# Kernel tuning notes

Hardware: AMD Instinct MI355X
Metric: run time of the kernel (lower is better)

## Reference

```python
import jax, jax.numpy as jnp
from jax import lax
import numpy as np

B, P, G, C = 16, 6000, 128, 10
PC_MIN = np.array([-54.0, -54.0, -5.0], np.float32)
PC_MAX = np.array([54.0, 54.0, 3.0], np.float32)
CENTER_RADIUS = 1.5
CANDIDATE_TOPK = 5
NUM_HEADS = 6
CLS_W, ALPHA, GAMMA = 2.0, 0.25, 2.0
REG_W, IOU_W = 0.25, 0.25
EPS = 1e-12
INF1, INF2 = 10000.0, 100000.0


def _aabb(boxes):
    # boxes: (N,7) [cx,cy,cz,dx,dy,dz,yaw] -> AABB (min,max) of the 8 rotated corners
    c, d, yaw = boxes[:, :3], boxes[:, 3:6], boxes[:, 6]
    ca, sa = jnp.abs(jnp.cos(yaw)), jnp.abs(jnp.sin(yaw))
    hx = 0.5 * (d[:, 0] * ca + d[:, 1] * sa)
    hy = 0.5 * (d[:, 0] * sa + d[:, 1] * ca)
    h = jnp.stack([hx, hy, 0.5 * d[:, 2]], -1)
    return c - h, c + h


def _iou3d(pred7, gt7):
    # axis-aligned 3D IoU over corner AABBs (reference stand-in for rotated BboxOverlaps3D)
    pmin, pmax = _aabb(pred7)
    gmin, gmax = _aabb(gt7)
    lo = jnp.maximum(pmin[:, None], gmin[None])   # (P,G,3)
    hi = jnp.minimum(pmax[:, None], gmax[None])
    inter = jnp.prod(jnp.maximum(hi - lo, 0.0), -1)
    vp = jnp.prod(pmax - pmin, -1)
    vg = jnp.prod(gmax - gmin, -1)
    return inter / (vp[:, None] + vg[None] - inter + 1e-7)


def _cost_matrix(pred_logits, pred_boxes, gt_boxes, gt_labels):
    # --- focal classification cost ---
    p = jax.nn.sigmoid(pred_logits)                                  # (P,C)
    neg = -jnp.log(1.0 - p + EPS) * (1.0 - ALPHA) * p ** GAMMA
    pos = -jnp.log(p + EPS) * ALPHA * (1.0 - p) ** GAMMA
    cls_cost = (pos - neg)[:, gt_labels] * CLS_W                     # (P,G)

    gt_norm = jnp.concatenate([gt_boxes[:, :3], jnp.log(gt_boxes[:, 3:6]),
                               jnp.sin(gt_boxes[:, 6:7]), jnp.cos(gt_boxes[:, 6:7])], -1)  # (G,8)
    reg_cost = jnp.abs(pred_boxes[:, None, :8] - gt_norm[None]).sum(-1) * REG_W

    # --- IoU cost on denormalized pred boxes ---
    yaw = jnp.arctan2(pred_boxes[:, 6], pred_boxes[:, 7])
    pred7 = jnp.concatenate([pred_boxes[:, :3], jnp.exp(pred_boxes[:, 3:6]), yaw[:, None]], -1)
    ious = _iou3d(pred7, gt_boxes)                                   # (P,G)
    iou_cost = -ious * IOU_W

    # --- in-gt-box / in-center geometric prior ---
    ctr = pred_boxes[:, :3]
    gmin, gmax = _aabb(gt_boxes)
    in_box = jnp.all((ctr[:, None] > gmin[None]) & (ctr[:, None] < gmax[None]), -1)  # (P,G)
    gc, gd = gt_boxes[:, :3], gt_boxes[:, 3:6]
    lo = gc - CENTER_RADIUS * gd
    hi = gc + CENTER_RADIUS * gd
    in_ctr = jnp.all((ctr[:, None] > lo[None]) & (ctr[:, None] < hi[None]), -1)
    valid = jnp.any(in_box, 1) | jnp.any(in_ctr, 1)                  # (P,)
    in_both = in_box & in_ctr

    cost = cls_cost + reg_cost + iou_cost + (~in_both).astype(cls_cost.dtype) * 100.0
    cost = cost + (~valid).astype(cls_cost.dtype)[:, None] * INF1
    return cost, ious, valid


def _assign(pred_logits, pred_boxes, gt_boxes, gt_labels, head_idx):
    cost, ious, valid = _cost_matrix(pred_logits, pred_boxes, gt_boxes, gt_labels)

    # dynamic-k per gt: sum of top-k ious minus head-schedule offset, truncated, min 1
    k = min(CANDIDATE_TOPK, P)
    topk_ious = lax.top_k(ious.T, k)[0]                              # (G,k)
    dyn = jnp.maximum((topk_ious.sum(1) - 0.5 * (NUM_HEADS - head_idx)).astype(jnp.int32), 1)

    # per-gt lowest-cost top-dyn selection via double argsort ranks
    ranks = jnp.argsort(jnp.argsort(cost, axis=0), axis=0)           # (P,G)
    matching = (ranks < dyn[None, :]).astype(cost.dtype)

    # priors matched to >1 gt: keep only the min-cost gt
    prior_mask = matching.sum(1) > 1
    onehot_min = jax.nn.one_hot(jnp.argmin(cost, 1), G, dtype=cost.dtype)
    matching = jnp.where(prior_mask[:, None], onehot_min, matching)

    rows = jnp.arange(P)

    def cond(s):
        i, cst, m = s
        return jnp.any(m.sum(0) == 0) & (i < G + 8)

    def body(s):
        i, cst, m = s
        cst = cst + (m.sum(1) > 0).astype(cst.dtype)[:, None] * INF2
        unmatched = m.sum(0) == 0                                    # (G,)
        pos = jnp.argmin(cst, 0)                                     # (G,) best prior per gt
        m = jnp.where((rows[:, None] == pos[None]) & unmatched[None], 1.0, m)
        over = jnp.any(m.sum(1) > 1)
        oh = jax.nn.one_hot(jnp.argmin(cst, 1), G, dtype=cst.dtype)
        m = jnp.where(over & prior_mask[:, None], oh, m)             # stale mask, as in torch source
        return i + 1, cst, m

    _, _, matching = lax.while_loop(cond, body, (jnp.int32(0), cost, matching))

    fg = matching.sum(1) > 0                                         # (P,) foreground mask
    matched = jnp.where(fg, jnp.argmax(matching, 1), -1).astype(jnp.int32)
    return fg, matched


def setup_inputs():
    key = jax.random.key(0)
    k1, k2, k3, k4, k5, k6, k7, k8 = jax.random.split(key, 8)
    pred_logits = jax.random.normal(k1, (B, P, C), jnp.float32)
    ctr = jax.random.uniform(k2, (B, P, 3), jnp.float32, jnp.array(PC_MIN), jnp.array(PC_MAX))
    logsz = jnp.log(jax.random.uniform(k3, (B, P, 3), jnp.float32, 1.0, 4.0))
    ang = jax.random.uniform(k4, (B, P, 1), jnp.float32, -np.pi, np.pi)
    vel = jax.random.normal(k5, (B, P, 2), jnp.float32)
    pred_boxes = jnp.concatenate([ctr, logsz, jnp.sin(ang), jnp.cos(ang), vel], -1)
    gctr = jax.random.uniform(k6, (B, G, 3), jnp.float32, jnp.array(PC_MIN), jnp.array(PC_MAX))
    gsz = jax.random.uniform(k7, (B, G, 3), jnp.float32, 1.0, 5.0)
    gyaw = jax.random.uniform(k8, (B, G, 1), jnp.float32, -np.pi, np.pi)
    gt_boxes = jnp.concatenate([gctr, gsz, gyaw], -1)
    gt_labels = jax.random.randint(jax.random.fold_in(key, 99), (B, G), 0, C)
    return {"pred_logits": pred_logits, "pred_boxes": pred_boxes,
            "gt_boxes": gt_boxes, "gt_labels": gt_labels, "head_idx": 5}


def reference(pred_logits, pred_boxes, gt_boxes, gt_labels, head_idx):
    f = lambda pl, pb, gb, gl: _assign(pl, pb, gb, gl, head_idx)
    fg, matched = jax.vmap(f)(pred_logits, pred_boxes, gt_boxes, gt_labels)
    return fg, matched
```

## Files before the change

### kernel.cpp

```cpp
#include <hip/hip_runtime.h>
#include <stdint.h>
#include <math.h>

#define NB 16
#define NP 6000
#define NG 128
#define NC 10
#define SELMAX 4
#define GSTR 24
#define PCH 2048
#define NCH 3
#define CPB 2
#define QITER 32
#define EPIW 128

typedef unsigned long long u64;
#define NBPs ((size_t)NB * NP)

__device__ __forceinline__ uint32_t fkey(float f) {
  uint32_t u = __float_as_uint(f);
  return (u & 0x80000000u) ? ~u : (u | 0x80000000u);
}
__device__ __forceinline__ float fkey_inv(uint32_t k) {
  uint32_t u = (k & 0x80000000u) ? (k & 0x7fffffffu) : ~k;
  return __uint_as_float(u);
}
__device__ __forceinline__ u64 shfl_xor_u64(u64 v, int m) {
  uint32_t lo = (uint32_t)v, hi = (uint32_t)(v >> 32);
  lo = (uint32_t)__shfl_xor((int)lo, m, 64);
  hi = (uint32_t)__shfl_xor((int)hi, m, 64);
  return ((u64)hi << 32) | lo;
}
__device__ __forceinline__ u64 block_min_u64(u64 v, u64* sred, int lane, int wid) {
  for (int o = 1; o < 64; o <<= 1) {
    u64 t = shfl_xor_u64(v, o);
    if (t < v) v = t;
  }
  __syncthreads();
  if (lane == 0) sred[wid] = v;
  __syncthreads();
  u64 r = sred[0];
  if (sred[1] < r) r = sred[1];
  if (sred[2] < r) r = sred[2];
  if (sred[3] < r) r = sred[3];
  return r;
}

__global__ __launch_bounds__(256) void prep_kernel(
    const float* __restrict__ gt_boxes,
    const int* __restrict__ gt_labels,
    const float* __restrict__ pred_logits,
    const float* __restrict__ pred_boxes,
    float* __restrict__ gtaux,
    float* __restrict__ paux,
    float* __restrict__ clst,
    int* __restrict__ rowcnt,
    int* __restrict__ rowassign,
    int* __restrict__ colcnt,
    int* __restrict__ wcount) {
#pragma clang fp contract(off)
  __shared__ float shg[NG * 12];
  const int b = blockIdx.y, tid = threadIdx.x;
  if (tid < NG) {
    const int g = tid;
    const float* gb = gt_boxes + ((size_t)b * NG + g) * 7;
    float cx = gb[0], cy = gb[1], cz = gb[2];
    float dx = gb[3], dy = gb[4], dz = gb[5];
    float yaw = gb[6];
    float cyw = cosf(yaw), syw = sinf(yaw);
    float ca = fabsf(cyw), sa = fabsf(syw);
    float hx = 0.5f * (dx * ca + dy * sa);
    float hy = 0.5f * (dx * sa + dy * ca);
    float hz = 0.5f * dz;
    float gmin0 = cx - hx, gmin1 = cy - hy, gmin2 = cz - hz;
    float gmax0 = cx + hx, gmax1 = cy + hy, gmax2 = cz + hz;
    float* s = &shg[g * 12];
    s[0] = gmin0; s[1] = gmin1; s[2] = gmin2;
    s[3] = gmax0; s[4] = gmax1; s[5] = gmax2;
    s[6] = cx - 1.5f * dx; s[7] = cy - 1.5f * dy; s[8] = cz - 1.5f * dz;
    s[9] = cx + 1.5f * dx; s[10] = cy + 1.5f * dy; s[11] = cz + 1.5f * dz;
    if (blockIdx.x == 0) {
      float vg = ((gmax0 - gmin0) * (gmax1 - gmin1)) * (gmax2 - gmin2);
      float* o = gtaux + ((size_t)b * NG + g) * GSTR;
      o[0] = gmin0; o[1] = gmin1; o[2] = gmin2;
      o[3] = gmax0; o[4] = gmax1; o[5] = gmax2;
      o[6] = s[6]; o[7] = s[7]; o[8] = s[8];
      o[9] = s[9]; o[10] = s[10]; o[11] = s[11];
      o[12] = cx; o[13] = cy; o[14] = cz;
      o[15] = logf(dx); o[16] = logf(dy); o[17] = logf(dz);
      o[18] = syw; o[19] = cyw;
      o[20] = vg;
      o[21] = __int_as_float(gt_labels[(size_t)b * NG + g]);
      o[22] = 0.0f; o[23] = 0.0f;
      colcnt[b * NG + g] = 0;
      if (b == 0 && g == 0) wcount[0] = 0;
    }
  }
  __syncthreads();
  const int p = blockIdx.x * 256 + tid;
  if (p >= NP) return;
  const size_t idx = (size_t)b * NP + p;
  const float* lg = pred_logits + idx * NC;
  for (int c = 0; c < NC; ++c) {
    float x = lg[c];
    float pr = 1.0f / (1.0f + expf(-x));
    float neg = (-logf(1.0f - pr + 1e-12f) * 0.75f) * (pr * pr);
    float pos = (-logf(pr + 1e-12f) * 0.25f) * ((1.0f - pr) * (1.0f - pr));
    clst[(size_t)c * NBPs + idx] = (pos - neg) * 2.0f;
  }
  const float* bx = pred_boxes + idx * 10;
  float b0 = bx[0], b1 = bx[1], b2 = bx[2], b3 = bx[3], b4 = bx[4];
  float b5 = bx[5], b6 = bx[6], b7 = bx[7];
  float yaw = atan2f(b6, b7);
  float d0 = expf(b3), d1 = expf(b4), d2 = expf(b5);
  float ca = fabsf(cosf(yaw)), sa = fabsf(sinf(yaw));
  float hx = 0.5f * (d0 * ca + d1 * sa);
  float hy = 0.5f * (d0 * sa + d1 * ca);
  float hz = 0.5f * d2;
  float pmin0 = b0 - hx, pmin1 = b1 - hy, pmin2 = b2 - hz;
  float pmax0 = b0 + hx, pmax1 = b1 + hy, pmax2 = b2 + hz;
  int valid = 0;
  for (int g = 0; g < NG; ++g) {
    const float* s = &shg[g * 12];
    bool inb = (b0 > s[0]) && (b0 < s[3]) && (b1 > s[1]) && (b1 < s[4]) &&
               (b2 > s[2]) && (b2 < s[5]);
    bool inc = (b0 > s[6]) && (b0 < s[9]) && (b1 > s[7]) && (b1 < s[10]) &&
               (b2 > s[8]) && (b2 < s[11]);
    if (inb || inc) { valid = 1; break; }
  }
  float* o = paux + idx * 16;
  o[0] = b0; o[1] = b1; o[2] = b2; o[3] = b3;
  o[4] = b4; o[5] = b5; o[6] = b6; o[7] = b7;
  o[8] = pmin0; o[9] = pmin1; o[10] = pmin2;
  o[11] = pmax0; o[12] = pmax1; o[13] = pmax2;
  o[14] = ((pmax0 - pmin0) * (pmax1 - pmin1)) * (pmax2 - pmin2);
  o[15] = valid ? 0.0f : 10000.0f;
  rowcnt[idx] = 0;
  rowassign[idx] = 0x7fffffff;
}

struct GTp {
  float gmin0, gmin1, gmin2, gmax0, gmax1, gmax2;
  float lo0, lo1, lo2, hi0, hi1, hi2;
  float gtn0, gtn1, gtn2, gtn3, gtn4, gtn5, gtn6, gtn7;
  float vg;
  int label;
};
__device__ __forceinline__ GTp load_gt(const float* __restrict__ gtaux,
                                       int b, int g) {
  const float* ga = gtaux + ((size_t)b * NG + g) * GSTR;
  GTp t;
  t.gmin0 = ga[0]; t.gmin1 = ga[1]; t.gmin2 = ga[2];
  t.gmax0 = ga[3]; t.gmax1 = ga[4]; t.gmax2 = ga[5];
  t.lo0 = ga[6]; t.lo1 = ga[7]; t.lo2 = ga[8];
  t.hi0 = ga[9]; t.hi1 = ga[10]; t.hi2 = ga[11];
  t.gtn0 = ga[12]; t.gtn1 = ga[13]; t.gtn2 = ga[14]; t.gtn3 = ga[15];
  t.gtn4 = ga[16]; t.gtn5 = ga[17]; t.gtn6 = ga[18]; t.gtn7 = ga[19];
  t.vg = ga[20];
  t.label = __float_as_int(ga[21]);
  return t;
}

__device__ __forceinline__ float cost_base(
    float b0, float b1, float b2, float b3, float b4, float b5, float b6,
    float b7, float pmin0, float pmin1, float pmin2, float pmax0, float pmax1,
    float pmax2, float vp, float cls, const GTp& t, float* iou_out) {
#pragma clang fp contract(off)
  float r = fabsf(b0 - t.gtn0);
  r = r + fabsf(b1 - t.gtn1);
  r = r + fabsf(b2 - t.gtn2);
  r = r + fabsf(b3 - t.gtn3);
  r = r + fabsf(b4 - t.gtn4);
  r = r + fabsf(b5 - t.gtn5);
  r = r + fabsf(b6 - t.gtn6);
  r = r + fabsf(b7 - t.gtn7);
  float reg = r * 0.25f;
  float li0 = fmaxf(pmin0, t.gmin0), li1 = fmaxf(pmin1, t.gmin1),
        li2 = fmaxf(pmin2, t.gmin2);
  float hj0 = fminf(pmax0, t.gmax0), hj1 = fminf(pmax1, t.gmax1),
        hj2 = fminf(pmax2, t.gmax2);
  float e0 = fmaxf(hj0 - li0, 0.0f), e1 = fmaxf(hj1 - li1, 0.0f),
        e2 = fmaxf(hj2 - li2, 0.0f);
  float inter = (e0 * e1) * e2;
  float iou = inter / (((vp + t.vg) - inter) + 1e-7f);
  bool inb = (b0 > t.gmin0) && (b0 < t.gmax0) && (b1 > t.gmin1) &&
             (b1 < t.gmax1) && (b2 > t.gmin2) && (b2 < t.gmax2);
  bool inc = (b0 > t.lo0) && (b0 < t.hi0) && (b1 > t.lo1) && (b1 < t.hi1) &&
             (b2 > t.lo2) && (b2 < t.hi2);
  *iou_out = iou;
  return ((cls + reg) + (-(iou * 0.25f))) + ((inb && inc) ? 0.0f : 100.0f);
}

__global__ __launch_bounds__(256) void stage1_kernel(
    const float* __restrict__ paux,
    const float* __restrict__ clst,
    const float* __restrict__ gtaux,
    float* __restrict__ iou5,
    u64* __restrict__ ck) {
#pragma clang fp contract(off)
  const int n = blockIdx.x;
  const int orig = (n & 7) * 384 + (n >> 3);
  const int b = orig / 192;
  const int rem = orig - b * 192;
  const int gq = rem / NCH;
  const int ch = rem - gq * NCH;
  const int g0 = gq * CPB;
  const int tid = threadIdx.x;
  const int lane = tid & 63, wid = tid >> 6;

  __shared__ uint32_t kiouL[CPB][PCH];
  __shared__ uint32_t kcostL[CPB][PCH];

  GTp t0 = load_gt(gtaux, b, g0);
  GTp t1 = load_gt(gtaux, b, g0 + 1);
  const size_t rowbase = (size_t)b * NP;
  const uint32_t PAD_I = fkey(-INFINITY);
  const uint32_t PAD_C = fkey(INFINITY);

  for (int j = 0; j < PCH / 256; ++j) {
    const int pl = j * 256 + tid;
    const int p = ch * PCH + pl;
    uint32_t ki0 = PAD_I, ki1 = PAD_I, kc0 = PAD_C, kc1 = PAD_C;
    if (p < NP) {
      const size_t idx = rowbase + p;
      const float4* pa = (const float4*)(paux + idx * 16);
      float4 A = pa[0], B = pa[1], C = pa[2], D = pa[3];
      float cls0 = clst[(size_t)t0.label * NBPs + idx];
      float cls1 = clst[(size_t)t1.label * NBPs + idx];
      float iou0, iou1;
      float c0 = cost_base(A.x, A.y, A.z, A.w, B.x, B.y, B.z, B.w,
                           C.x, C.y, C.z, C.w, D.x, D.y, D.z,
                           cls0, t0, &iou0);
      float c1 = cost_base(A.x, A.y, A.z, A.w, B.x, B.y, B.z, B.w,
                           C.x, C.y, C.z, C.w, D.x, D.y, D.z,
                           cls1, t1, &iou1);
      ki0 = fkey(iou0); kc0 = fkey(c0 + D.w);
      ki1 = fkey(iou1); kc1 = fkey(c1 + D.w);
    }
    kiouL[0][pl] = ki0;
    kiouL[1][pl] = ki1;
    kcostL[0][pl] = kc0;
    kcostL[1][pl] = kc1;
  }
  __syncthreads();

  const int c = wid >> 1;
  const int col = b * NG + g0 + c;
  const unsigned gbase = (unsigned)(ch * PCH);

  if ((wid & 1) == 0) {
    uint32_t a0 = 0, a1 = 0, a2 = 0, a3 = 0, a4 = 0;
    for (int q = 0; q < QITER; ++q) {
      uint32_t k = kiouL[c][q * 64 + lane];
      if (k > a4) {
        a4 = k;
        if (a4 > a3) { uint32_t t = a4; a4 = a3; a3 = t; }
        if (a3 > a2) { uint32_t t = a3; a3 = a2; a2 = t; }
        if (a2 > a1) { uint32_t t = a2; a2 = a1; a1 = t; }
        if (a1 > a0) { uint32_t t = a1; a1 = a0; a0 = t; }
      }
    }
    int hp = 0;
    for (int k = 0; k < 5; ++k) {
      uint32_t cand = (hp == 0) ? a0 : (hp == 1) ? a1 : (hp == 2) ? a2
                    : (hp == 3) ? a3 : (hp == 4) ? a4 : 0u;
      u64 key = ((u64)cand << 32) | (unsigned)lane;
      u64 r = key;
      for (int o = 1; o < 64; o <<= 1) {
        u64 t = shfl_xor_u64(r, o);
        if (t > r) r = t;
      }
      if (lane == 0)
        iou5[(size_t)col * 16 + ch * 5 + k] = fkey_inv((uint32_t)(r >> 32));
      if (r == key) hp++;
    }
  } else {
    u64 c0 = ~0ull, c1 = ~0ull, c2 = ~0ull, c3 = ~0ull;
    for (int q = 0; q < QITER; ++q) {
      const int pl = q * 64 + lane;
      u64 key = ((u64)kcostL[c][pl] << 32) | (u64)(gbase + (unsigned)pl);
      if (key < c3) {
        c3 = key;
        if (c3 < c2) { u64 t = c3; c3 = c2; c2 = t; }
        if (c2 < c1) { u64 t = c2; c2 = c1; c1 = t; }
        if (c1 < c0) { u64 t = c1; c1 = c0; c0 = t; }
      }
    }
    int hp = 0;
    for (int k = 0; k < 4; ++k) {
      u64 cand = (hp == 0) ? c0 : (hp == 1) ? c1 : (hp == 2) ? c2
               : (hp == 3) ? c3 : ~0ull;
      u64 r = cand;
      for (int o = 1; o < 64; o <<= 1) {
        u64 t = shfl_xor_u64(r, o);
        if (t < r) r = t;
      }
      if (lane == 0) ck[(size_t)col * 16 + ch * 4 + k] = r;
      if (r == cand) hp++;
    }
  }
}

__global__ __launch_bounds__(256) void stage2_kernel(
    const float* __restrict__ iou5,
    const u64* __restrict__ ck,
    const int* __restrict__ head_ptr,
    int* __restrict__ colsel,
    int* __restrict__ rowcnt,
    int* __restrict__ rowassign,
    int* __restrict__ wlist,
    int* __restrict__ wcount) {
#pragma clang fp contract(off)
  const int col = blockIdx.x * 256 + threadIdx.x;
  if (col >= NB * NG) return;
  const int b = col / NG, g = col - b * NG;
  const float* ip = iou5 + (size_t)col * 16;
  float m0 = -INFINITY, m1 = -INFINITY, m2 = -INFINITY, m3 = -INFINITY,
        m4 = -INFINITY;
  for (int i = 0; i < 5 * NCH; ++i) {
    float v = ip[i];
    if (v > m4) {
      m4 = v;
      if (m4 > m3) { float t = m4; m4 = m3; m3 = t; }
      if (m3 > m2) { float t = m3; m3 = m2; m2 = t; }
      if (m2 > m1) { float t = m2; m2 = m1; m1 = t; }
      if (m1 > m0) { float t = m1; m1 = m0; m0 = t; }
    }
  }
  float sum5 = ((((m0 + m1) + m2) + m3) + m4);
  float adj = sum5 - 0.5f * (float)(6 - head_ptr[0]);
  int dyn = (int)adj;
  if (dyn < 1) dyn = 1;
  if (dyn > SELMAX) dyn = SELMAX;

  const u64* kp = ck + (size_t)col * 16;
  u64 s0 = ~0ull, s1 = ~0ull, s2 = ~0ull, s3 = ~0ull;
  for (int i = 0; i < SELMAX * NCH; ++i) {
    u64 k = kp[i];
    if (k < s3) {
      s3 = k;
      if (s3 < s2) { u64 t = s3; s3 = s2; s2 = t; }
      if (s2 < s1) { u64 t = s2; s2 = s1; s1 = t; }
      if (s1 < s0) { u64 t = s1; s1 = s0; s0 = t; }
    }
  }
  const size_t rowbase = (size_t)b * NP;
  int pk[4];
  pk[0] = (int)(s0 & 0xffffffffu);
  pk[1] = (int)(s1 & 0xffffffffu);
  pk[2] = (int)(s2 & 0xffffffffu);
  pk[3] = (int)(s3 & 0xffffffffu);
  for (int k = 0; k < SELMAX; ++k) {
    int sel = (k < dyn) ? pk[k] : -1;
    colsel[(size_t)col * SELMAX + k] = sel;
    if (sel >= 0) {
      int old = atomicAdd(&rowcnt[rowbase + sel], 1);
      if (old == 1) {
        int slot = atomicAdd(wcount, 1);
        wlist[slot] = (int)(rowbase + sel);
      }
      atomicMin(&rowassign[rowbase + sel], g);
    }
  }
}

__global__ __launch_bounds__(256) void epi_kernel(
    const float* __restrict__ paux,
    const float* __restrict__ clst,
    const float* __restrict__ gtaux,
    const int* __restrict__ colsel,
    const int* __restrict__ rowcnt,
    const int* __restrict__ wlist,
    const int* __restrict__ wcount,
    int* __restrict__ rowminArr,
    int* __restrict__ colcnt) {
#pragma clang fp contract(off)
  const int tid = threadIdx.x;
  if (blockIdx.x >= EPIW) {
    const int col = (blockIdx.x - EPIW) * 256 + tid;
    if (col < NB * NG) {
      const int b = col / NG;
      int cnt = 0;
      const size_t cb = (size_t)col * SELMAX;
      for (int k = 0; k < SELMAX; ++k) {
        int s = colsel[cb + k];
        if (s >= 0 && rowcnt[(size_t)b * NP + s] == 1) cnt++;
      }
      if (cnt) atomicAdd(&colcnt[col], cnt);
    }
    return;
  }
  const int lane = tid & 63, wid = tid >> 6;
  const int wavesTotal = EPIW * 4;
  const int wave = blockIdx.x * 4 + wid;
  const int n = wcount[0];
  for (int e = wave; e < n; e += wavesTotal) {
    const int idx = wlist[e];
    const int b = idx / NP;
    const float4* pa = (const float4*)(paux + (size_t)idx * 16);
    float4 A = pa[0], Bq = pa[1], Cq = pa[2], Dq = pa[3];
    const float pen = Dq.w;
    u64 best = ~0ull;
    for (int h = 0; h < 2; ++h) {
      const int g = h * 64 + lane;
      GTp t = load_gt(gtaux, b, g);
      float cls = clst[(size_t)t.label * NBPs + idx];
      float iou;
      float cc = cost_base(A.x, A.y, A.z, A.w, Bq.x, Bq.y, Bq.z, Bq.w,
                           Cq.x, Cq.y, Cq.z, Cq.w, Dq.x, Dq.y, Dq.z,
                           cls, t, &iou);
      u64 key = ((u64)fkey(cc + pen) << 32) | (unsigned)g;
      if (key < best) best = key;
    }
    for (int o = 1; o < 64; o <<= 1) {
      u64 t = shfl_xor_u64(best, o);
      if (t < best) best = t;
    }
    if (lane == 0) {
      const int bg = (int)(best & 0xffffffffu);
      rowminArr[idx] = bg;
      atomicAdd(&colcnt[b * NG + bg], 1);
    }
  }
}

__global__ __launch_bounds__(256) void fixup_kernel(
    const float* __restrict__ paux,
    const float* __restrict__ clst,
    const float* __restrict__ gtaux,
    const int* __restrict__ colcnt,
    const int* __restrict__ rowcnt,
    int* __restrict__ rowassign) {
#pragma clang fp contract(off)
  const int g = blockIdx.x, b = blockIdx.y, tid = threadIdx.x;
  if (colcnt[b * NG + g] != 0) return;
  const int lane = tid & 63, wid = tid >> 6;
  const size_t rowbase = (size_t)b * NP;
  GTp t = load_gt(gtaux, b, g);
  u64 best = ~0ull;
  for (int p = tid; p < NP; p += 256) {
    const size_t idx = rowbase + p;
    if (rowcnt[idx] == 0) {
      const float4* pa = (const float4*)(paux + idx * 16);
      float4 A = pa[0], Bq = pa[1], Cq = pa[2], Dq = pa[3];
      float cls = clst[(size_t)t.label * NBPs + idx];
      float iou;
      float cc = cost_base(A.x, A.y, A.z, A.w, Bq.x, Bq.y, Bq.z, Bq.w,
                           Cq.x, Cq.y, Cq.z, Cq.w, Dq.x, Dq.y, Dq.z,
                           cls, t, &iou);
      u64 key = ((u64)fkey(cc + Dq.w) << 32) | (unsigned)p;
      if (key < best) best = key;
    }
  }
  __shared__ u64 sred[4];
  u64 rr = block_min_u64(best, sred, lane, wid);
  if (tid == 0) {
    int pos = (int)(rr & 0xffffffffu);
    atomicMin(&rowassign[rowbase + pos], g);
  }
}

__global__ void output_kernel(const int* __restrict__ rowcnt,
                              const int* __restrict__ rowassign,
                              const int* __restrict__ rowminArr,
                              int* __restrict__ out) {
  const int i = blockIdx.x * 256 + threadIdx.x;
  if (i >= (int)NBPs) return;
  int rc = rowcnt[i];
  int fg, m;
  if (rc == 0) {
    int ra = rowassign[i];
    if (ra == 0x7fffffff) { fg = 0; m = -1; }
    else { fg = 1; m = ra; }
  } else if (rc == 1) {
    fg = 1; m = rowassign[i];
  } else {
    fg = 1; m = rowminArr[i];
  }
  out[i] = fg;
  out[NBPs + i] = m;
}

extern "C" void kernel_launch(void* const* d_in, const int* in_sizes, int n_in,
                              void* d_out, int out_size, void* d_ws, size_t ws_size,
                              hipStream_t stream) {
  const float* pred_logits = (const float*)d_in[0];
  const float* pred_boxes = (const float*)d_in[1];
  const float* gt_boxes = (const float*)d_in[2];
  const int* gt_labels = (const int*)d_in[3];
  const int* head = (const int*)d_in[4];
  (void)in_sizes; (void)n_in; (void)out_size; (void)ws_size;

  char* w = (char*)d_ws;
  size_t off = 0;
  auto alloc = [&](size_t bytes) -> void* {
    void* p = w + off;
    off += (bytes + 255) & ~(size_t)255;
    return p;
  };
  float* paux = (float*)alloc((size_t)NB * NP * 16 * 4);
  float* clst = (float*)alloc((size_t)NC * NB * NP * 4);
  float* gtaux = (float*)alloc((size_t)NB * NG * GSTR * 4);
  float* iou5 = (float*)alloc((size_t)NB * NG * 16 * 4);
  u64* ck = (u64*)alloc((size_t)NB * NG * 16 * 8);
  int* colsel = (int*)alloc((size_t)NB * NG * SELMAX * 4);
  int* rowcnt = (int*)alloc((size_t)NB * NP * 4);
  int* rowassign = (int*)alloc((size_t)NB * NP * 4);
  int* rowminArr = (int*)alloc((size_t)NB * NP * 4);
  int* colcnt = (int*)alloc((size_t)NB * NG * 4);
  int* wlist = (int*)alloc((size_t)NB * NP * 4);
  int* wcount = (int*)alloc(256);

  int* out = (int*)d_out;
  dim3 blk(256);
  prep_kernel<<<dim3((NP + 255) / 256, NB), blk, 0, stream>>>(
      gt_boxes, gt_labels, pred_logits, pred_boxes, gtaux, paux, clst,
      rowcnt, rowassign, colcnt, wcount);
  stage1_kernel<<<dim3(NB * (NG / CPB) * NCH), blk, 0, stream>>>(
      paux, clst, gtaux, iou5, ck);
  stage2_kernel<<<dim3((NB * NG + 255) / 256), blk, 0, stream>>>(
      iou5, ck, head, colsel, rowcnt, rowassign, wlist, wcount);
  epi_kernel<<<dim3(EPIW + 8), blk, 0, stream>>>(
      paux, clst, gtaux, colsel, rowcnt, wlist, wcount, rowminArr, colcnt);
  fixup_kernel<<<dim3(NG, NB), blk, 0, stream>>>(
      paux, clst, gtaux, colcnt, rowcnt, rowassign);
  output_kernel<<<dim3(((int)NBPs + 255) / 256), blk, 0, stream>>>(
      rowcnt, rowassign, rowminArr, out);
}
```

Before: 123.2 us.

## Fuse stage1 and stage2 into one select kernel with register top-k

Merges the chunked per-column top-k kernel and the follow-up selection kernel into one kernel that covers all predictions per column pair. Each thread keeps running top-5 IoU and top-4 cost lists in registers rather than staging keys in shared memory, then does wave reductions and a final merge across the four waves. This removes one kernel launch, the intermediate global buffers and the shared-memory staging. In exchange the grid shrinks from 3072 to 1024 blocks, each with a longer serial loop, and per-thread register pressure rises.

```diff
diff --git a/kernel.cpp b/kernel.cpp
--- a/kernel.cpp
+++ b/kernel.cpp
@@ -8,10 +8,8 @@
 #define NC 10
 #define SELMAX 4
 #define GSTR 24
-#define PCH 2048
-#define NCH 3
 #define CPB 2
-#define QITER 32
+#define QN 24
 #define EPIW 128
 
 typedef unsigned long long u64;
@@ -44,6 +42,58 @@
   if (sred[2] < r) r = sred[2];
   if (sred[3] < r) r = sred[3];
   return r;
+}
+
+__device__ __forceinline__ void ins5max(uint32_t& a0, uint32_t& a1, uint32_t& a2,
+                                        uint32_t& a3, uint32_t& a4, uint32_t k) {
+  if (k > a4) {
+    a4 = k;
+    if (a4 > a3) { uint32_t t = a4; a4 = a3; a3 = t; }
+    if (a3 > a2) { uint32_t t = a3; a3 = a2; a2 = t; }
+    if (a2 > a1) { uint32_t t = a2; a2 = a1; a1 = t; }
+    if (a1 > a0) { uint32_t t = a1; a1 = a0; a0 = t; }
+  }
+}
+__device__ __forceinline__ void ins4min(u64& c0, u64& c1, u64& c2, u64& c3, u64 k) {
+  if (k < c3) {
+    c3 = k;
+    if (c3 < c2) { u64 t = c3; c3 = c2; c2 = t; }
+    if (c2 < c1) { u64 t = c2; c2 = c1; c1 = t; }
+    if (c1 < c0) { u64 t = c1; c1 = c0; c0 = t; }
+  }
+}
+__device__ __forceinline__ void wave_top5_iou(uint32_t a0, uint32_t a1,
+                                              uint32_t a2, uint32_t a3,
+                                              uint32_t a4, int lane,
+                                              float* dst) {
+  int hp = 0;
+  for (int k = 0; k < 5; ++k) {
+    uint32_t cand = (hp == 0) ? a0 : (hp == 1) ? a1 : (hp == 2) ? a2
+                  : (hp == 3) ? a3 : (hp == 4) ? a4 : 0u;
+    u64 key = ((u64)cand << 32) | (unsigned)lane;
+    u64 r = key;
+    for (int o = 1; o < 64; o <<= 1) {
+      u64 t = shfl_xor_u64(r, o);
+      if (t > r) r = t;
+    }
+    if (lane == 0) dst[k] = fkey_inv((uint32_t)(r >> 32));
+    if (r == key) hp++;
+  }
+}
+__device__ __forceinline__ void wave_top4_cost(u64 c0, u64 c1, u64 c2, u64 c3,
+                                               int lane, u64* dst) {
+  int hp = 0;
+  for (int k = 0; k < 4; ++k) {
+    u64 cand = (hp == 0) ? c0 : (hp == 1) ? c1 : (hp == 2) ? c2
+             : (hp == 3) ? c3 : ~0ull;
+    u64 r = cand;
+    for (int o = 1; o < 64; o <<= 1) {
+      u64 t = shfl_xor_u64(r, o);
+      if (t < r) r = t;
+    }
+    if (lane == 0) dst[k] = r;
+    if (r == cand) hp++;
+  }
 }
 
 __global__ __launch_bounds__(256) void prep_kernel(
@@ -191,36 +241,35 @@
   return ((cls + reg) + (-(iou * 0.25f))) + ((inb && inc) ? 0.0f : 100.0f);
 }
 
-__global__ __launch_bounds__(256) void stage1_kernel(
+__global__ __launch_bounds__(256) void select_kernel(
     const float* __restrict__ paux,
     const float* __restrict__ clst,
     const float* __restrict__ gtaux,
-    float* __restrict__ iou5,
-    u64* __restrict__ ck) {
+    const int* __restrict__ head_ptr,
+    int* __restrict__ colsel,
+    int* __restrict__ rowcnt,
+    int* __restrict__ rowassign,
+    int* __restrict__ wlist,
+    int* __restrict__ wcount) {
 #pragma clang fp contract(off)
   const int n = blockIdx.x;
-  const int orig = (n & 7) * 384 + (n >> 3);
-  const int b = orig / 192;
-  const int rem = orig - b * 192;
-  const int gq = rem / NCH;
-  const int ch = rem - gq * NCH;
-  const int g0 = gq * CPB;
+  const int orig = (n & 7) * 128 + (n >> 3);
+  const int b = orig >> 6;
+  const int g0 = (orig & 63) * CPB;
   const int tid = threadIdx.x;
   const int lane = tid & 63, wid = tid >> 6;
 
-  __shared__ uint32_t kiouL[CPB][PCH];
-  __shared__ uint32_t kcostL[CPB][PCH];
-
-  GTp t0 = load_gt(gtaux, b, g0);
-  GTp t1 = load_gt(gtaux, b, g0 + 1);
+  const GTp t0 = load_gt(gtaux, b, g0);
+  const GTp t1 = load_gt(gtaux, b, g0 + 1);
   const size_t rowbase = (size_t)b * NP;
-  const uint32_t PAD_I = fkey(-INFINITY);
-  const uint32_t PAD_C = fkey(INFINITY);
-
-  for (int j = 0; j < PCH / 256; ++j) {
-    const int pl = j * 256 + tid;
-    const int p = ch * PCH + pl;
-    uint32_t ki0 = PAD_I, ki1 = PAD_I, kc0 = PAD_C, kc1 = PAD_C;
+
+  uint32_t i0a = 0, i0b = 0, i0c = 0, i0d = 0, i0e = 0;
+  uint32_t i1a = 0, i1b = 0, i1c = 0, i1d = 0, i1e = 0;
+  u64 k0a = ~0ull, k0b = ~0ull, k0c = ~0ull, k0d = ~0ull;
+  u64 k1a = ~0ull, k1b = ~0ull, k1c = ~0ull, k1d = ~0ull;
+
+  for (int q = 0; q < QN; ++q) {
+    const int p = q * 256 + tid;
     if (p < NP) {
       const size_t idx = rowbase + p;
       const float4* pa = (const float4*)(paux + idx * 16);
@@ -234,132 +283,79 @@
       float c1 = cost_base(A.x, A.y, A.z, A.w, B.x, B.y, B.z, B.w,
                            C.x, C.y, C.z, C.w, D.x, D.y, D.z,
                            cls1, t1, &iou1);
-      ki0 = fkey(iou0); kc0 = fkey(c0 + D.w);
-      ki1 = fkey(iou1); kc1 = fkey(c1 + D.w);
-    }
-    kiouL[0][pl] = ki0;
-    kiouL[1][pl] = ki1;
-    kcostL[0][pl] = kc0;
-    kcostL[1][pl] = kc1;
-  }
+      ins5max(i0a, i0b, i0c, i0d, i0e, fkey(iou0));
+      ins5max(i1a, i1b, i1c, i1d, i1e, fkey(iou1));
+      ins4min(k0a, k0b, k0c, k0d, ((u64)fkey(c0 + D.w) << 32) | (unsigned)p);
+      ins4min(k1a, k1b, k1c, k1d, ((u64)fkey(c1 + D.w) << 32) | (unsigned)p);
+    }
+  }
+
+  __shared__ float iouF[4][CPB][5];
+  __shared__ u64 ckF[4][CPB][4];
+  wave_top5_iou(i0a, i0b, i0c, i0d, i0e, lane, &iouF[wid][0][0]);
+  wave_top5_iou(i1a, i1b, i1c, i1d, i1e, lane, &iouF[wid][1][0]);
+  wave_top4_cost(k0a, k0b, k0c, k0d, lane, &ckF[wid][0][0]);
+  wave_top4_cost(k1a, k1b, k1c, k1d, lane, &ckF[wid][1][0]);
   __syncthreads();
 
-  const int c = wid >> 1;
-  const int col = b * NG + g0 + c;
-  const unsigned gbase = (unsigned)(ch * PCH);
-
-  if ((wid & 1) == 0) {
-    uint32_t a0 = 0, a1 = 0, a2 = 0, a3 = 0, a4 = 0;
-    for (int q = 0; q < QITER; ++q) {
-      uint32_t k = kiouL[c][q * 64 + lane];
-      if (k > a4) {
-        a4 = k;
-        if (a4 > a3) { uint32_t t = a4; a4 = a3; a3 = t; }
-        if (a3 > a2) { uint32_t t = a3; a3 = a2; a2 = t; }
-        if (a2 > a1) { uint32_t t = a2; a2 = a1; a1 = t; }
-        if (a1 > a0) { uint32_t t = a1; a1 = a0; a0 = t; }
+  if (tid < CPB) {
+    const int c = tid;
+    const int g = g0 + c;
+    const int col = b * NG + g;
+    float m0 = -INFINITY, m1 = -INFINITY, m2 = -INFINITY, m3 = -INFINITY,
+          m4 = -INFINITY;
+    for (int w = 0; w < 4; ++w) {
+      for (int j = 0; j < 5; ++j) {
+        float v = iouF[w][c][j];
+        if (v > m4) {
+          m4 = v;
+          if (m4 > m3) { float t = m4; m4 = m3; m3 = t; }
+          if (m3 > m2) { float t = m3; m3 = m2; m2 = t; }
+          if (m2 > m1) { float t = m2; m2 = m1; m1 = t; }
+          if (m1 > m0) { float t = m1; m1 = m0; m0 = t; }
+        }
       }
     }
-    int hp = 0;
-    for (int k = 0; k < 5; ++k) {
-      uint32_t cand = (hp == 0) ? a0 : (hp == 1) ? a1 : (hp == 2) ? a2
-                    : (hp == 3) ? a3 : (hp == 4) ? a4 : 0u;
-      u64 key = ((u64)cand << 32) | (unsigned)lane;
-      u64 r = key;
-      for (int o = 1; o < 64; o <<= 1) {
-        u64 t = shfl_xor_u64(r, o);
-        if (t > r) r = t;
+    float sum5 = ((((m0 + m1) + m2) + m3) + m4);
+    float adj = sum5 - 0.5f * (float)(6 - head_ptr[0]);
+    int dyn = (int)adj;
+    if (dyn < 1) dyn = 1;
+    if (dyn > SELMAX) dyn = SELMAX;
+    u64 s0 = ~0ull, s1 = ~0ull, s2 = ~0ull, s3 = ~0ull;
+    for (int w = 0; w < 4; ++w) {
+      for (int j = 0; j < 4; ++j) {
+        u64 k = ckF[w][c][j];
+        if (k < s3) {
+          s3 = k;
+          if (s3 < s2) { u64 t = s3; s3 = s2; s2 = t; }
+          if (s2 < s1) { u64 t = s2; s2 = s1; s1 = t; }
+          if (s1 < s0) { u64 t = s1; s1 = s0; s0 = t; }
+        }
       }
-      if (lane == 0)
-        iou5[(size_t)col * 16 + ch * 5 + k] = fkey_inv((uint32_t)(r >> 32));
-      if (r == key) hp++;
-    }
-  } else {
-    u64 c0 = ~0ull, c1 = ~0ull, c2 = ~0ull, c3 = ~0ull;
-    for (int q = 0; q < QITER; ++q) {
-      const int pl = q * 64 + lane;
-      u64 key = ((u64)kcostL[c][pl] << 32) | (u64)(gbase + (unsigned)pl);
-      if (key < c3) {
-        c3 = key;
-        if (c3 < c2) { u64 t = c3; c3 = c2; c2 = t; }
-        if (c2 < c1) { u64 t = c2; c2 = c1; c1 = t; }
-        if (c1 < c0) { u64 t = c1; c1 = c0; c0 = t; }
+    }
+    int pk0 = (int)(s0 & 0xffffffffu);
+    int pk1 = (int)(s1 & 0xffffffffu);
+    int pk2 = (int)(s2 & 0xffffffffu);
+    int pk3 = (int)(s3 & 0xffffffffu);
+    int sel0 = (dyn > 0) ? pk0 : -1;
+    int sel1 = (dyn > 1) ? pk1 : -1;
+    int sel2 = (dyn > 2) ? pk2 : -1;
+    int sel3 = (dyn > 3) ? pk3 : -1;
+    colsel[(size_t)col * SELMAX + 0] = sel0;
+    colsel[(size_t)col * SELMAX + 1] = sel1;
+    colsel[(size_t)col * SELMAX + 2] = sel2;
+    colsel[(size_t)col * SELMAX + 3] = sel3;
+    int sels[4] = {sel0, sel1, sel2, sel3};
+    for (int k = 0; k < SELMAX; ++k) {
+      int sel = sels[k];
+      if (sel >= 0) {
+        int old = atomicAdd(&rowcnt[rowbase + sel], 1);
+        if (old == 1) {
+          int slot = atomicAdd(wcount, 1);
+          wlist[slot] = (int)(rowbase + sel);
+        }
+        atomicMin(&rowassign[rowbase + sel], g);
       }
-    }
-    int hp = 0;
-    for (int k = 0; k < 4; ++k) {
-      u64 cand = (hp == 0) ? c0 : (hp == 1) ? c1 : (hp == 2) ? c2
-               : (hp == 3) ? c3 : ~0ull;
-      u64 r = cand;
-      for (int o = 1; o < 64; o <<= 1) {
-        u64 t = shfl_xor_u64(r, o);
-        if (t < r) r = t;
-      }
-      if (lane == 0) ck[(size_t)col * 16 + ch * 4 + k] = r;
-      if (r == cand) hp++;
-    }
-  }
-}
-
-__global__ __launch_bounds__(256) void stage2_kernel(
-    const float* __restrict__ iou5,
-    const u64* __restrict__ ck,
-    const int* __restrict__ head_ptr,
-    int* __restrict__ colsel,
-    int* __restrict__ rowcnt,
-    int* __restrict__ rowassign,
-    int* __restrict__ wlist,
-    int* __restrict__ wcount) {
-#pragma clang fp contract(off)
-  const int col = blockIdx.x * 256 + threadIdx.x;
-  if (col >= NB * NG) return;
-  const int b = col / NG, g = col - b * NG;
-  const float* ip = iou5 + (size_t)col * 16;
-  float m0 = -INFINITY, m1 = -INFINITY, m2 = -INFINITY, m3 = -INFINITY,
-        m4 = -INFINITY;
-  for (int i = 0; i < 5 * NCH; ++i) {
-    float v = ip[i];
-    if (v > m4) {
-      m4 = v;
-      if (m4 > m3) { float t = m4; m4 = m3; m3 = t; }
-      if (m3 > m2) { float t = m3; m3 = m2; m2 = t; }
-      if (m2 > m1) { float t = m2; m2 = m1; m1 = t; }
-      if (m1 > m0) { float t = m1; m1 = m0; m0 = t; }
-    }
-  }
-  float sum5 = ((((m0 + m1) + m2) + m3) + m4);
-  float adj = sum5 - 0.5f * (float)(6 - head_ptr[0]);
-  int dyn = (int)adj;
-  if (dyn < 1) dyn = 1;
-  if (dyn > SELMAX) dyn = SELMAX;
-
-  const u64* kp = ck + (size_t)col * 16;
-  u64 s0 = ~0ull, s1 = ~0ull, s2 = ~0ull, s3 = ~0ull;
-  for (int i = 0; i < SELMAX * NCH; ++i) {
-    u64 k = kp[i];
-    if (k < s3) {
-      s3 = k;
-      if (s3 < s2) { u64 t = s3; s3 = s2; s2 = t; }
-      if (s2 < s1) { u64 t = s2; s2 = s1; s1 = t; }
-      if (s1 < s0) { u64 t = s1; s1 = s0; s0 = t; }
-    }
-  }
-  const size_t rowbase = (size_t)b * NP;
-  int pk[4];
-  pk[0] = (int)(s0 & 0xffffffffu);
-  pk[1] = (int)(s1 & 0xffffffffu);
-  pk[2] = (int)(s2 & 0xffffffffu);
-  pk[3] = (int)(s3 & 0xffffffffu);
-  for (int k = 0; k < SELMAX; ++k) {
-    int sel = (k < dyn) ? pk[k] : -1;
-    colsel[(size_t)col * SELMAX + k] = sel;
-    if (sel >= 0) {
-      int old = atomicAdd(&rowcnt[rowbase + sel], 1);
-      if (old == 1) {
-        int slot = atomicAdd(wcount, 1);
-        wlist[slot] = (int)(rowbase + sel);
-      }
-      atomicMin(&rowassign[rowbase + sel], g);
     }
   }
 }
@@ -501,8 +497,6 @@
   float* paux = (float*)alloc((size_t)NB * NP * 16 * 4);
   float* clst = (float*)alloc((size_t)NC * NB * NP * 4);
   float* gtaux = (float*)alloc((size_t)NB * NG * GSTR * 4);
-  float* iou5 = (float*)alloc((size_t)NB * NG * 16 * 4);
-  u64* ck = (u64*)alloc((size_t)NB * NG * 16 * 8);
   int* colsel = (int*)alloc((size_t)NB * NG * SELMAX * 4);
   int* rowcnt = (int*)alloc((size_t)NB * NP * 4);
   int* rowassign = (int*)alloc((size_t)NB * NP * 4);
@@ -516,10 +510,8 @@
   prep_kernel<<<dim3((NP + 255) / 256, NB), blk, 0, stream>>>(
       gt_boxes, gt_labels, pred_logits, pred_boxes, gtaux, paux, clst,
       rowcnt, rowassign, colcnt, wcount);
-  stage1_kernel<<<dim3(NB * (NG / CPB) * NCH), blk, 0, stream>>>(
-      paux, clst, gtaux, iou5, ck);
-  stage2_kernel<<<dim3((NB * NG + 255) / 256), blk, 0, stream>>>(
-      iou5, ck, head, colsel, rowcnt, rowassign, wlist, wcount);
+  select_kernel<<<dim3(NB * NG / CPB), blk, 0, stream>>>(
+      paux, clst, gtaux, head, colsel, rowcnt, rowassign, wlist, wcount);
   epi_kernel<<<dim3(EPIW + 8), blk, 0, stream>>>(
       paux, clst, gtaux, colsel, rowcnt, wlist, wcount, rowminArr, colcnt);
   fixup_kernel<<<dim3(NG, NB), blk, 0, stream>>>(
```

After: 117.2 us. -4.9%, faster.
